# Performance work log

Hardware: AMD Instinct MI355X
Metric: run time of the kernel (lower is better)

## Reference

```python
import jax, jax.numpy as jnp
import numpy as np


def setup_inputs() -> dict:
    key = jax.random.key(0)
    ks = jax.random.split(key, 9)
    N, C, SY, SX = 256, 128, 11, 25
    DM, DC, D = 64, 64, 128
    return {
        "f_t_global": jax.random.normal(ks[0], (N, D), dtype=jnp.float32),
        "x_t_local": jax.random.normal(ks[1], (N, C, SY, SX), dtype=jnp.float32),
        "x_t_prev_local": jax.random.normal(ks[2], (N, C, SY, SX), dtype=jnp.float32),
        "m_t": jax.random.normal(ks[3], (N, DM), dtype=jnp.float32),
        "m_t_prev": jax.random.normal(ks[4], (N, DM), dtype=jnp.float32),
        "c_t": jax.random.normal(ks[5], (N, DC), dtype=jnp.float32),
        "c_t_prev": jax.random.normal(ks[6], (N, DC), dtype=jnp.float32),
        "W_join": jax.random.normal(ks[7], (C + DM + DC, D), dtype=jnp.float32) * 0.05,
        "b_join": jax.random.normal(ks[8], (D,), dtype=jnp.float32) * 0.05,
    }


def reference(f_t_global, x_t_local, x_t_prev_local, m_t, m_t_prev, c_t, c_t_prev, W_join, b_join):
    N, C, SY, SX = x_t_local.shape
    P = SY * SX
    DM = m_t.shape[1]
    # join_obs(local, m, c) = concat([local, m, c]) @ W_join + b_join, split for efficiency
    Wl = W_join[:C]                 # [C, D]
    Wm = W_join[C:C + DM]           # [DM, D]
    Wc = W_join[C + DM:]            # [DC, D]
    # [N, C, SY, SX] -> [P, N, C]: all spatial positions batched at once
    loc_t = x_t_local.reshape(N, C, P).transpose(2, 0, 1)
    loc_p = x_t_prev_local.reshape(N, C, P).transpose(2, 0, 1)
    bias_t = m_t @ Wm + c_t @ Wc + b_join             # [N, D], shared across positions
    bias_p = m_t_prev @ Wm + c_t_prev @ Wc + b_join   # [N, D]
    positive = jnp.einsum('pnc,cd->pnd', loc_p, Wl) + bias_p[None]  # [P, N, D]
    pred_loc = jnp.einsum('pnc,cd->pnd', loc_t, Wl) + bias_t[None]  # [P, N, D]

    # loss1: global prediction vs per-position prev-local positives
    logits1 = jnp.einsum('nd,pmd->pnm', f_t_global, positive)   # [P, N, N]
    # loss2: per-position current-local vs per-position prev-local
    logits2 = jnp.einsum('pnd,pmd->pnm', pred_loc, positive)    # [P, N, N]

    def mean_infonce(logits):
        # cross_entropy(logits, arange(N)) averaged over batch, then over positions
        lse = jax.nn.logsumexp(logits, axis=-1)            # [P, N]
        diag = jnp.diagonal(logits, axis1=1, axis2=2)      # [P, N]
        return jnp.mean(lse - diag)

    loss1 = mean_infonce(logits1)
    loss2 = mean_infonce(logits2)
    return loss1 + loss2
```

## Files before the change

kernel.cpp:

```cpp
#include <hip/hip_runtime.h>

#define Nn 256
#define Cc 128
#define Pp 275
#define Dd 128

typedef unsigned int u32;
typedef unsigned short u16;
typedef float f32x4 __attribute__((ext_vector_type(4)));
typedef short bf16x8 __attribute__((ext_vector_type(8)));

__device__ __forceinline__ float bf2f(u16 h) {
    return __uint_as_float(((u32)h) << 16);
}
__device__ __forceinline__ u16 f2bf(float f) {
    u32 u = __float_as_uint(f);
    return (u16)((u + 0x7fffu + ((u >> 16) & 1u)) >> 16);
}

__global__ __launch_bounds__(256) void bias_kernel(
    const float* __restrict__ m_t, const float* __restrict__ m_p,
    const float* __restrict__ c_t, const float* __restrict__ c_p,
    const float* __restrict__ W, const float* __restrict__ b,
    const float* __restrict__ f,
    float* __restrict__ bias_t, float* __restrict__ bias_p,
    u16* __restrict__ f_bf, u16* __restrict__ WlT)
{
    int idx = blockIdx.x * 256 + threadIdx.x;
    int n = idx >> 7, d = idx & 127;
    float at = 0.f, ap = 0.f;
#pragma unroll 8
    for (int k = 0; k < 64; ++k) {
        float wm = W[(128 + k) * 128 + d];
        float wc = W[(192 + k) * 128 + d];
        at = fmaf(m_t[n * 64 + k], wm, at);
        at = fmaf(c_t[n * 64 + k], wc, at);
        ap = fmaf(m_p[n * 64 + k], wm, ap);
        ap = fmaf(c_p[n * 64 + k], wc, ap);
    }
    float bb = b[d];
    bias_t[idx] = at + bb;
    bias_p[idx] = ap + bb;
    f_bf[idx] = f2bf(f[idx]);
    if (idx < 16384) {
        int dd = idx >> 7, cc = idx & 127;
        WlT[idx] = f2bf(W[cc * 128 + dd]);
    }
}

__global__ __launch_bounds__(512) void join_dbuf_kernel(
    const float* __restrict__ x_t, const float* __restrict__ x_p,
    const u16* __restrict__ WlT,
    const float* __restrict__ bias_t, const float* __restrict__ bias_p,
    u16* __restrict__ pred, u16* __restrict__ pos)
{
    __shared__ u16 wlds[128 * 128];
    __shared__ u16 xlds[2][2][16 * 128];
    const int tid = threadIdx.x;
    const int half = blockIdx.x;
    const int n = blockIdx.y;
    const int w = tid >> 6;
    const int l = tid & 63;
    const int g = l >> 4;

    {
        const uint4* src = reinterpret_cast<const uint4*>(WlT);
#pragma unroll
        for (int it = 0; it < 4; ++it) {
            int j = tid + 512 * it;
            int row = j >> 4;
            int colb = (j & 15) << 4;
            uint4 v = src[j];
            *reinterpret_cast<uint4*>((char*)wlds + row * 256 + (colb ^ ((row & 7) << 4))) = v;
        }
    }

    const int sq = tid & 255;
    const int spass = tid >> 8;
    const int sc0 = (sq >> 2) * 2;
    const int sp4 = (sq & 3) << 2;
    const float* sx = (spass ? x_p : x_t) + (size_t)n * (Cc * Pp);

    const int cpass = w & 1;
    const int dt0 = w >> 1;
    const float* bias = cpass ? bias_p : bias_t;
    u16* outp = cpass ? pos : pred;
    const float bv0 = bias[n * 128 + dt0 * 16 + (l & 15)];
    const float bv1 = bias[n * 128 + (dt0 + 4) * 16 + (l & 15)];

    {
        const int ch = half * 9;
        const int p0 = (ch < 17) ? ch * 16 : 259;
        const float* a = sx + (size_t)sc0 * Pp + p0 + sp4;
        f32x4 t0 = *reinterpret_cast<const f32x4*>(a);
        f32x4 t1 = *reinterpret_cast<const f32x4*>(a + Pp);
#pragma unroll
        for (int e = 0; e < 4; ++e) {
            const int row = sp4 + e;
            u32 pk = (u32)f2bf(t0[e]) | ((u32)f2bf(t1[e]) << 16);
            *reinterpret_cast<u32*>((char*)&xlds[0][spass][0]
                + row * 256 + ((sc0 * 2) ^ ((row & 7) << 4))) = pk;
        }
    }
    __syncthreads();

    int ib = 0;
    for (int tt = 0; tt < 9; ++tt) {
        const int ch = half * 9 + tt;
        const int p0 = (ch < 17) ? ch * 16 : 259;

        f32x4 t0, t1;
        const bool have = (tt < 8);
        if (have) {
            const int chn = ch + 1;
            const int pn0 = (chn < 17) ? chn * 16 : 259;
            const float* a = sx + (size_t)sc0 * Pp + pn0 + sp4;
            t0 = *reinterpret_cast<const f32x4*>(a);
            t1 = *reinterpret_cast<const f32x4*>(a + Pp);
        }

        const char* ab = (const char*)&xlds[ib][cpass][0];
        const int arow = l & 15;
        bf16x8 A[4];
#pragma unroll
        for (int kk = 0; kk < 4; ++kk)
            A[kk] = *reinterpret_cast<const bf16x8*>(
                ab + arow * 256 + ((kk * 64 + g * 16) ^ ((arow & 7) << 4)));

#pragma unroll
        for (int i = 0; i < 2; ++i) {
            const int dt = dt0 + i * 4;
            bf16x8 B[4];
            const int row = dt * 16 + (l & 15);
#pragma unroll
            for (int kk = 0; kk < 4; ++kk) {
                int cbyte = kk * 64 + (g << 4);
                B[kk] = *reinterpret_cast<const bf16x8*>(
                    (const char*)wlds + row * 256 + (cbyte ^ ((row & 7) << 4)));
            }
            f32x4 acc = {0.f, 0.f, 0.f, 0.f};
#pragma unroll
            for (int kk = 0; kk < 4; ++kk)
                acc = __builtin_amdgcn_mfma_f32_16x16x32_bf16(A[kk], B[kk], acc, 0, 0, 0);
            const int d = dt * 16 + (l & 15);
            const float bv = i ? bv1 : bv0;
#pragma unroll
            for (int r = 0; r < 4; ++r) {
                const int p = p0 + g * 4 + r;
                outp[((size_t)p * Nn + n) * Dd + d] = f2bf(acc[r] + bv);
            }
        }

        if (have) {
#pragma unroll
            for (int e = 0; e < 4; ++e) {
                const int row = sp4 + e;
                u32 pk = (u32)f2bf(t0[e]) | ((u32)f2bf(t1[e]) << 16);
                *reinterpret_cast<u32*>((char*)&xlds[ib ^ 1][spass][0]
                    + row * 256 + ((sc0 * 2) ^ ((row & 7) << 4))) = pk;
            }
        }
        __syncthreads();
        ib ^= 1;
    }
}

__global__ __launch_bounds__(512) void logits_mfma_kernel(
    const u16* __restrict__ f_bf,
    const u16* __restrict__ pred, const u16* __restrict__ pos,
    float* __restrict__ partial)
{
    __shared__ u16 lds[Nn * Dd];
    const int tid = threadIdx.x;
    const int sel = blockIdx.x;
    const int p = blockIdx.y;
    const int w = tid >> 6;
    const int l = tid & 63;
    const int r0 = w * 32;

    {
        const uint4* src = reinterpret_cast<const uint4*>(pos + (size_t)p * (Nn * Dd));
#pragma unroll
        for (int it = 0; it < 8; ++it) {
            int j = tid + 512 * it;
            int row = j >> 4;
            int colb = (j & 15) << 4;
            uint4 v = src[j];
            *reinterpret_cast<uint4*>((char*)lds + row * 256 + (colb ^ ((row & 7) << 4))) = v;
        }
    }

    const u16* Abase = sel ? (pred + (size_t)p * (Nn * Dd)) : f_bf;
    bf16x8 A[2][4];
    {
        const int arow = l & 15;
        const int acol = (l >> 4) << 4;
#pragma unroll
        for (int rt = 0; rt < 2; ++rt)
#pragma unroll
            for (int kk = 0; kk < 4; ++kk) {
                const char* ap = (const char*)Abase
                               + (size_t)(r0 + rt * 16 + arow) * 256 + kk * 64 + acol;
                A[rt][kk] = *reinterpret_cast<const bf16x8*>(ap);
            }
    }

    __syncthreads();

    const float L2E = 1.4426950408889634f;
    float s_[2][4];
    float dg[2][4];
#pragma unroll
    for (int rt = 0; rt < 2; ++rt)
#pragma unroll
        for (int r = 0; r < 4; ++r) { s_[rt][r] = 0.f; dg[rt][r] = 0.f; }

    const int mcol = l & 15;
    const int bcol = (l >> 4) << 4;

    for (int ct = 0; ct < 16; ++ct) {
        bf16x8 B[4];
        const int mrow = ct * 16 + mcol;
#pragma unroll
        for (int kk = 0; kk < 4; ++kk) {
            int cb = kk * 64 + bcol;
            B[kk] = *reinterpret_cast<const bf16x8*>(
                (const char*)lds + mrow * 256 + (cb ^ ((mrow & 7) << 4)));
        }
#pragma unroll
        for (int rt = 0; rt < 2; ++rt) {
            f32x4 acc = {0.f, 0.f, 0.f, 0.f};
#pragma unroll
            for (int kk = 0; kk < 4; ++kk)
                acc = __builtin_amdgcn_mfma_f32_16x16x32_bf16(A[rt][kk], B[kk], acc, 0, 0, 0);
            const bool isdg_ct = (ct == ((r0 >> 4) + rt));
#pragma unroll
            for (int r = 0; r < 4; ++r) {
                float v = acc[r];
                s_[rt][r] += __builtin_amdgcn_exp2f(fmaf(v, L2E, -64.f));
                if (isdg_ct && ((l & 15) == (((l >> 4) << 2) + r))) dg[rt][r] = v;
            }
        }
    }

    float local = 0.f;
#pragma unroll
    for (int rt = 0; rt < 2; ++rt)
#pragma unroll
        for (int r = 0; r < 4; ++r) {
            float s = s_[rt][r];
            s += __shfl_xor(s, 1);
            s += __shfl_xor(s, 2);
            s += __shfl_xor(s, 4);
            s += __shfl_xor(s, 8);
            if ((l & 15) == (((l >> 4) << 2) + r))
                local += 0.6931471805599453f * (64.f + __log2f(s)) - dg[rt][r];
        }

    __syncthreads();
    float* red = reinterpret_cast<float*>(lds);
    red[tid] = local;
    __syncthreads();
    for (int k = 256; k > 0; k >>= 1) {
        if (tid < k) red[tid] += red[tid + k];
        __syncthreads();
    }
    if (tid == 0) partial[p * 2 + sel] = red[0];
}

__global__ __launch_bounds__(256) void reduce_kernel(
    const float* __restrict__ partial, float* __restrict__ out)
{
    __shared__ float red[256];
    float s = 0.f;
    for (int i = threadIdx.x; i < 2 * Pp; i += 256) s += partial[i];
    red[threadIdx.x] = s;
    __syncthreads();
    for (int k = 128; k > 0; k >>= 1) {
        if (threadIdx.x < k) red[threadIdx.x] += red[threadIdx.x + k];
        __syncthreads();
    }
    if (threadIdx.x == 0) out[0] = red[0] * (1.0f / (Pp * (float)Nn));
}

extern "C" void kernel_launch(void* const* d_in, const int* in_sizes, int n_in,
                              void* d_out, int out_size, void* d_ws, size_t ws_size,
                              hipStream_t stream)
{
    const float* f   = (const float*)d_in[0];
    const float* x_t = (const float*)d_in[1];
    const float* x_p = (const float*)d_in[2];
    const float* m_t = (const float*)d_in[3];
    const float* m_p = (const float*)d_in[4];
    const float* c_t = (const float*)d_in[5];
    const float* c_p = (const float*)d_in[6];
    const float* W   = (const float*)d_in[7];
    const float* b   = (const float*)d_in[8];

    char* ws = (char*)d_ws;
    const size_t SLAB = (size_t)Pp * Nn * Dd;

    float* bias_t = (float*)ws;
    float* bias_p = bias_t + Nn * Dd;
    u16* f_bf = (u16*)(ws + 262144);
    u16* WlT  = f_bf + Nn * Dd;
    u16* pred = (u16*)(ws + 360448);
    u16* pos  = pred + SLAB;
    float* partial = (float*)(pos + SLAB);

    bias_kernel<<<dim3(Nn * Dd / 256), 256, 0, stream>>>(m_t, m_p, c_t, c_p, W, b, f,
                                                         bias_t, bias_p, f_bf, WlT);
    join_dbuf_kernel<<<dim3(2, Nn), 512, 0, stream>>>(x_t, x_p, WlT, bias_t, bias_p,
                                                      pred, pos);
    logits_mfma_kernel<<<dim3(2, Pp), 512, 0, stream>>>(f_bf, pred, pos, partial);
    reduce_kernel<<<1, 256, 0, stream>>>(partial, (float*)d_out);
}
```

Measured before the change: 68.37 us.

## Split logits kernel over column halves and add merge kernel for logsumexp

The logits kernel now splits each position's 256 target columns into two halves, so it launches twice as many blocks, each staging half the positive slab in LDS (32 KB instead of 64 KB). Per-row partial exp-sums and diagonal values go to workspace, and a new merge kernel adds the halves, takes the log and reduces per position. This is meant to raise occupancy and parallelism across the CUs. The cost is an extra kernel launch, extra global traffic for the partial sums, and each block still reloading its full A rows.

```diff
diff --git a/kernel.cpp b/kernel.cpp
--- a/kernel.cpp
+++ b/kernel.cpp
@@ -165,23 +165,25 @@
     }
 }
 
-__global__ __launch_bounds__(512) void logits_mfma_kernel(
+__global__ __launch_bounds__(512) void logits_part_kernel(
     const u16* __restrict__ f_bf,
     const u16* __restrict__ pred, const u16* __restrict__ pos,
-    float* __restrict__ partial)
-{
-    __shared__ u16 lds[Nn * Dd];
+    float* __restrict__ spart, float* __restrict__ dgarr)
+{
+    __shared__ u16 lds[128 * Dd];
     const int tid = threadIdx.x;
-    const int sel = blockIdx.x;
+    const int sel = blockIdx.x >> 1;
+    const int mhalf = blockIdx.x & 1;
     const int p = blockIdx.y;
     const int w = tid >> 6;
     const int l = tid & 63;
     const int r0 = w * 32;
 
     {
-        const uint4* src = reinterpret_cast<const uint4*>(pos + (size_t)p * (Nn * Dd));
-#pragma unroll
-        for (int it = 0; it < 8; ++it) {
+        const uint4* src = reinterpret_cast<const uint4*>(
+            pos + (size_t)p * (Nn * Dd) + (size_t)mhalf * 128 * Dd);
+#pragma unroll
+        for (int it = 0; it < 4; ++it) {
             int j = tid + 512 * it;
             int row = j >> 4;
             int colb = (j & 15) << 4;
@@ -218,9 +220,9 @@
     const int mcol = l & 15;
     const int bcol = (l >> 4) << 4;
 
-    for (int ct = 0; ct < 16; ++ct) {
+    for (int ctl = 0; ctl < 8; ++ctl) {
         bf16x8 B[4];
-        const int mrow = ct * 16 + mcol;
+        const int mrow = ctl * 16 + mcol;
 #pragma unroll
         for (int kk = 0; kk < 4; ++kk) {
             int cb = kk * 64 + bcol;
@@ -233,7 +235,7 @@
 #pragma unroll
             for (int kk = 0; kk < 4; ++kk)
                 acc = __builtin_amdgcn_mfma_f32_16x16x32_bf16(A[rt][kk], B[kk], acc, 0, 0, 0);
-            const bool isdg_ct = (ct == ((r0 >> 4) + rt));
+            const bool isdg_ct = ((mhalf * 8 + ctl) == ((r0 >> 4) + rt));
 #pragma unroll
             for (int r = 0; r < 4; ++r) {
                 float v = acc[r];
@@ -243,7 +245,9 @@
         }
     }
 
-    float local = 0.f;
+    float* sp = spart + (((size_t)(sel * Pp + p) * 2 + mhalf) << 8);
+    float* dp = dgarr + (((size_t)(sel * Pp + p)) << 8);
+    const bool owns_dg = ((w >> 2) == mhalf);
 #pragma unroll
     for (int rt = 0; rt < 2; ++rt)
 #pragma unroll
@@ -253,19 +257,33 @@
             s += __shfl_xor(s, 2);
             s += __shfl_xor(s, 4);
             s += __shfl_xor(s, 8);
-            if ((l & 15) == (((l >> 4) << 2) + r))
-                local += 0.6931471805599453f * (64.f + __log2f(s)) - dg[rt][r];
-        }
-
+            if ((l & 15) == (((l >> 4) << 2) + r)) {
+                const int n = r0 + rt * 16 + ((l >> 4) << 2) + r;
+                sp[n] = s;
+                if (owns_dg) dp[n] = dg[rt][r];
+            }
+        }
+}
+
+__global__ __launch_bounds__(256) void merge_kernel(
+    const float* __restrict__ spart, const float* __restrict__ dgarr,
+    float* __restrict__ partial)
+{
+    __shared__ float red[256];
+    const int sel = blockIdx.x;
+    const int p = blockIdx.y;
+    const int n = threadIdx.x;
+    const size_t base = ((size_t)(sel * Pp + p) * 2) << 8;
+    float s = spart[base + n] + spart[base + 256 + n];
+    float dgv = dgarr[(((size_t)(sel * Pp + p)) << 8) + n];
+    float val = 0.6931471805599453f * (64.f + __log2f(s)) - dgv;
+    red[n] = val;
     __syncthreads();
-    float* red = reinterpret_cast<float*>(lds);
-    red[tid] = local;
-    __syncthreads();
-    for (int k = 256; k > 0; k >>= 1) {
-        if (tid < k) red[tid] += red[tid + k];
+    for (int k = 128; k > 0; k >>= 1) {
+        if (n < k) red[n] += red[n + k];
         __syncthreads();
     }
-    if (tid == 0) partial[p * 2 + sel] = red[0];
+    if (n == 0) partial[sel * Pp + p] = red[0];
 }
 
 __global__ __launch_bounds__(256) void reduce_kernel(
@@ -307,11 +325,14 @@
     u16* pred = (u16*)(ws + 360448);
     u16* pos  = pred + SLAB;
     float* partial = (float*)(pos + SLAB);
+    float* spart   = partial + 2 * Pp;
+    float* dgarr   = spart + (size_t)2 * Pp * 2 * 256;
 
     bias_kernel<<<dim3(Nn * Dd / 256), 256, 0, stream>>>(m_t, m_p, c_t, c_p, W, b, f,
                                                          bias_t, bias_p, f_bf, WlT);
     join_dbuf_kernel<<<dim3(2, Nn), 512, 0, stream>>>(x_t, x_p, WlT, bias_t, bias_p,
                                                       pred, pos);
-    logits_mfma_kernel<<<dim3(2, Pp), 512, 0, stream>>>(f_bf, pred, pos, partial);
+    logits_part_kernel<<<dim3(4, Pp), 512, 0, stream>>>(f_bf, pred, pos, spart, dgarr);
+    merge_kernel<<<dim3(2, Pp), 256, 0, stream>>>(spart, dgarr, partial);
     reduce_kernel<<<1, 256, 0, stream>>>(partial, (float*)d_out);
 }
```

Measured after the change: 67.47 us. Within noise of the previous version (-1.3%).
